# Performance work log

Measured on AMD Instinct MI355X. Metric: run time of the kernel, lower is better.

Reference implementation:

```python
import jax, jax.numpy as jnp
import numpy as np

B, S, F = 4096, 128, 8
H1, H2 = 64, 32


def setup_inputs() -> dict:
    key = jax.random.key(0)
    ks = jax.random.split(key, 12)
    rn = lambda k, shape, scale: jax.random.normal(k, shape, dtype=jnp.float32) * scale
    return {
        "x": rn(ks[0], (B, S, F), 1.0),
        "time": jax.random.uniform(ks[1], (B, 1), dtype=jnp.float32),
        # linear_combine: (S*F + 1) -> S*F
        "W_combine": rn(ks[2], (S * F, S * F + 1), 1.0 / np.sqrt(S * F + 1)),
        "b_combine": jnp.zeros((S * F,), jnp.float32),
        # LSTM layer 1 (bias=False), gate order i,f,g,o like torch
        "W_ih1": rn(ks[3], (4 * H1, F), 1.0 / np.sqrt(H1)),
        "W_hh1": rn(ks[4], (4 * H1, H1), 1.0 / np.sqrt(H1)),
        # LSTM layer 2 (bias=True)
        "W_ih2": rn(ks[5], (4 * H2, H1), 1.0 / np.sqrt(H2)),
        "W_hh2": rn(ks[6], (4 * H2, H2), 1.0 / np.sqrt(H2)),
        "b_ih2": rn(ks[7], (4 * H2,), 0.05),
        "b_hh2": rn(ks[8], (4 * H2,), 0.05),
        # l_linear_supervised: (H2*S) -> 1
        "W_out": rn(ks[9], (1, H2 * S), 1.0 / np.sqrt(H2 * S)),
        "b_out": jnp.zeros((1,), jnp.float32),
    }


def _lstm(x, W_ih, W_hh, b):
    """batch_first LSTM, zero initial state. x: [B,S,D] -> hidden seq [B,S,H]."""
    Bq = x.shape[0]
    H = W_hh.shape[1]
    # precompute input contribution for all timesteps: [B,S,4H]
    xg = jnp.einsum('bsd,gd->bsg', x, W_ih) + b

    def step(carry, xg_t):
        h, c = carry
        g = xg_t + h @ W_hh.T
        i, f, gg, o = jnp.split(g, 4, axis=-1)  # torch gate order i,f,g,o
        c = jax.nn.sigmoid(f) * c + jax.nn.sigmoid(i) * jnp.tanh(gg)
        h = jax.nn.sigmoid(o) * jnp.tanh(c)
        return (h, c), h

    h0 = jnp.zeros((Bq, H), x.dtype)
    (_, _), hs = jax.lax.scan(step, (h0, h0), jnp.swapaxes(xg, 0, 1))
    return jnp.swapaxes(hs, 0, 1)


def reference(x, time, W_combine, b_combine, W_ih1, W_hh1, W_ih2, W_hh2,
              b_ih2, b_hh2, W_out, b_out):
    Bq = x.shape[0]
    # future_time_as_input == 1 branch: flatten, append time, linear + relu
    xf = jnp.concatenate([x.reshape(Bq, -1), time.reshape(Bq, -1)], axis=1)
    xf = jax.nn.relu(xf @ W_combine.T + b_combine)
    x1 = xf.reshape(Bq, S, F)
    h1 = _lstm(x1, W_ih1, W_hh1, jnp.zeros((4 * H1,), x.dtype))  # [B,S,64]
    h2 = _lstm(h1, W_ih2, W_hh2, b_ih2 + b_hh2)                   # [B,S,32]
    return h2.reshape(Bq, -1) @ W_out.T + b_out                   # [B,1]
```

## Files before the change

### kernel.cpp

```cpp
#include <hip/hip_runtime.h>
#include <math.h>


typedef _Float16 f16x8 __attribute__((ext_vector_type(8)));
typedef float f32x4 __attribute__((ext_vector_type(4)));

union H8 { uint4 q; _Float16 h[8]; f16x8 v; };

#define MF(A, B, C) __builtin_amdgcn_mfma_f32_16x16x32_f16(A, B, C, 0, 0, 0)
#define LOG2E 1.44269504f

__device__ __forceinline__ float sigm_pre(float y) {
  return __builtin_amdgcn_rcpf(1.f + __builtin_amdgcn_exp2f(-y));
}
__device__ __forceinline__ float tanh_pre(float y) {
  return 1.f - 2.f * __builtin_amdgcn_rcpf(1.f + __builtin_amdgcn_exp2f(y + y));
}
__device__ __forceinline__ float tanh_raw(float c) {
  return 1.f - 2.f * __builtin_amdgcn_rcpf(1.f + __builtin_amdgcn_exp2f(c * 2.88539008f));
}
__device__ __forceinline__ unsigned pkrtz(float a, float b) {
  return __builtin_bit_cast(unsigned, __builtin_amdgcn_cvt_pkrtz(a, b));
}

#define CROW 72

__global__ __launch_bounds__(256, 2) void combine_mfma(
    const float* __restrict__ x, const float* __restrict__ tme,
    const float* __restrict__ Wc, const float* __restrict__ bc,
    unsigned* __restrict__ x1u)
{
  __shared__ __align__(16) _Float16 sA[128][CROW];
  __shared__ __align__(16) _Float16 sB[64][CROW];
  __shared__ float sT[128];
  __shared__ float sWl[64];
  __shared__ float sBc[64];
  _Float16 (*Cst)[CROW] = sA;

  const int tid = threadIdx.x;
  const int lane = tid & 63;
  const int w = tid >> 6;
  const int r = lane & 15, grp = lane >> 4;
  const int M0 = blockIdx.y * 128, N0 = blockIdx.x * 64;

  if (tid < 128) sT[tid] = tme[M0 + tid];
  else if (tid < 192) sWl[tid - 128] = Wc[(size_t)(N0 + tid - 128) * 1025 + 1024];
  else sBc[tid - 192] = bc[N0 + tid - 192];

  f32x4 acc[2][4];
#pragma unroll
  for (int i = 0; i < 2; ++i)
#pragma unroll
    for (int j = 0; j < 4; ++j) acc[i][j] = f32x4{0.f, 0.f, 0.f, 0.f};

  for (int kt = 0; kt < 1024; kt += 64) {
#pragma unroll
    for (int i = 0; i < 8; ++i) {
      int idx = tid + i * 256;
      int row = idx >> 4, kq = idx & 15;
      float4 v = *(const float4*)&x[(size_t)(M0 + row) * 1024 + kt + kq * 4];
      *(uint2*)&sA[row][kq * 4] = uint2{pkrtz(v.x, v.y), pkrtz(v.z, v.w)};
    }
#pragma unroll
    for (int i = 0; i < 4; ++i) {
      int idx = tid + i * 256;
      int row = idx >> 4, kq = idx & 15;
      float4 v = *(const float4*)&Wc[(size_t)(N0 + row) * 1025 + kt + kq * 4];
      *(uint2*)&sB[row][kq * 4] = uint2{pkrtz(v.x, v.y), pkrtz(v.z, v.w)};
    }
    __syncthreads();

    H8 af[2][2], bf[4][2];
#pragma unroll
    for (int i = 0; i < 2; ++i)
#pragma unroll
      for (int c = 0; c < 2; ++c)
        af[i][c].q = *(const uint4*)&sA[w * 32 + i * 16 + r][c * 32 + grp * 8];
#pragma unroll
    for (int j = 0; j < 4; ++j)
#pragma unroll
      for (int c = 0; c < 2; ++c)
        bf[j][c].q = *(const uint4*)&sB[j * 16 + r][c * 32 + grp * 8];
#pragma unroll
    for (int i = 0; i < 2; ++i)
#pragma unroll
      for (int j = 0; j < 4; ++j) {
        acc[i][j] = MF(af[i][0].v, bf[j][0].v, acc[i][j]);
        acc[i][j] = MF(af[i][1].v, bf[j][1].v, acc[i][j]);
      }
    __syncthreads();
  }

#pragma unroll
  for (int i = 0; i < 2; ++i) {
#pragma unroll
    for (int j = 0; j < 4; ++j) {
      int n = j * 16 + r;
      float wl = sWl[n], bv = sBc[n];
#pragma unroll
      for (int q = 0; q < 4; ++q) {
        int mm = w * 32 + i * 16 + 4 * grp + q;
        float v = acc[i][j][q] + sT[mm] * wl + bv;
        Cst[mm][n] = (_Float16)fmaxf(v, 0.f);
      }
    }
  }
  __syncthreads();
#pragma unroll
  for (int i = 0; i < 4; ++i) {
    int idx = tid + i * 256;
    int row = idx >> 3, c8 = idx & 7;
    uint4 v = *(const uint4*)&Cst[row][c8 * 8];
    *(uint4*)&x1u[(size_t)(M0 + row) * 512 + (N0 >> 1) + c8 * 4] = v;
  }
}

#define ROW1 72
#define ROW2 40

__global__ __launch_bounds__(512, 2) void lstm_fused_mfma(
    const unsigned* __restrict__ x1u,
    const float* __restrict__ Wih1, const float* __restrict__ Whh1,
    const float* __restrict__ Wih2, const float* __restrict__ Whh2,
    const float* __restrict__ bih2, const float* __restrict__ bhh2,
    const float* __restrict__ Wout, const float* __restrict__ bout,
    float* __restrict__ out)
{
  __shared__ __align__(16) unsigned sxw[128 * 16 * 4];
  __shared__ float sWoT[32 * 132];
  __shared__ __align__(16) unsigned short sh1[2][16][ROW1];
  __shared__ __align__(16) unsigned short sh2[2][16][ROW2];
  __shared__ float sOut[8][16];

  const int tid = threadIdx.x;
  const int lane = tid & 63;
  const int w = tid >> 6;
  const int vw = w >> 1;
  const int wsub = w & 1;
  const int col = lane & 15;
  const int grp = lane >> 4;
  const int b0 = blockIdx.x * 16;

  const int m1 = col >> 2, g1 = col & 3;
  f16x8 A1h[2][2];
  f16x8 A1x[2];
#pragma unroll
  for (int jj = 0; jj < 2; ++jj) {
    const int wr = g1 * 64 + vw * 16 + 4 * m1 + (2 * wsub + jj);
#pragma unroll
    for (int c = 0; c < 2; ++c) {
      H8 f;
#pragma unroll
      for (int q = 0; q < 8; ++q)
        f.h[q] = (_Float16)(Whh1[wr * 64 + c * 32 + grp * 8 + q] * LOG2E);
      A1h[jj][c] = f.v;
    }
    H8 fx;
#pragma unroll
    for (int q = 0; q < 8; ++q)
      fx.h[q] = (grp == 0) ? (_Float16)(Wih1[wr * 8 + q] * LOG2E) : (_Float16)0.f;
    A1x[jj] = fx.v;
  }
  f16x8 A2[3];
  const int u = 2 * vw + wsub;
  {
    const int wr = g1 * 32 + 4 * u + m1;
#pragma unroll
    for (int c = 0; c < 3; ++c) {
      H8 f;
#pragma unroll
      for (int q = 0; q < 8; ++q) {
        float wv = (c < 2) ? Wih2[wr * 64 + c * 32 + grp * 8 + q]
                           : Whh2[wr * 32 + grp * 8 + q];
        f.h[q] = (_Float16)(wv * LOG2E);
      }
      A2[c] = f.v;
    }
  }
  const int h2o = 4 * u + grp;
  f32x4 b2q;
#pragma unroll
  for (int r = 0; r < 4; ++r)
    b2q[r] = (bih2[r * 32 + h2o] + bhh2[r * 32 + h2o]) * LOG2E;
  const f32x4 zq = {0.f, 0.f, 0.f, 0.f};

  for (int idx = tid; idx < 4096; idx += 512) {
    int t = idx >> 5, h = idx & 31;
    sWoT[h * 132 + t] = Wout[idx];
  }
  {
    unsigned short* z = &sh1[0][0][0];
    for (int i2 = tid; i2 < 2 * 16 * ROW1; i2 += 512) z[i2] = 0;
    unsigned short* z2 = &sh2[0][0][0];
    for (int i2 = tid; i2 < 2 * 16 * ROW2; i2 += 512) z2[i2] = 0;
  }
  for (int idx = tid; idx < 16 * 512; idx += 512) {
    int bb = idx >> 9, rem = idx & 511;
    int t = rem >> 2, pr = rem & 3;
    sxw[t * 64 + bb * 4 + pr] = x1u[(size_t)(b0 + bb) * 512 + rem];
  }
  __syncthreads();

  float c1a = 0.f, c1b = 0.f, c2 = 0.f, accO = 0.f;

#define PHASE(T, CUR, DO_L1, DO_L2)                                            \
  {                                                                            \
    H8 s0, s1, s2;                                                             \
    s0.q = *(const uint4*)&sh1[CUR][col][grp * 8];                             \
    s1.q = *(const uint4*)&sh1[CUR][col][32 + grp * 8];                        \
    s2.q = *(const uint4*)&sh2[CUR][col][grp * 8];                             \
    if (DO_L2) {                                                               \
      const float won = sWoT[h2o * 132 + (T) - 1];                             \
      f32x4 a = MF(A2[2], s2.v, b2q);                                          \
      a = MF(A2[0], s0.v, a);                                                  \
      a = MF(A2[1], s1.v, a);                                                  \
      float ig = sigm_pre(a[0]), fg = sigm_pre(a[1]);                          \
      float tg = tanh_pre(a[2]), og = sigm_pre(a[3]);                          \
      float cc = fg * c2 + ig * tg;                                            \
      c2 = cc;                                                                 \
      float hn = og * tanh_raw(cc);                                            \
      accO = fmaf(hn, won, accO);                                              \
      *(_Float16*)&sh2[(CUR) ^ 1][col][h2o] = (_Float16)hn;                    \
    }                                                                          \
    if (DO_L1) {                                                               \
      H8 sx;                                                                   \
      sx.q = *(const uint4*)&sxw[(T) * 64 + col * 4];                          \
      f32x4 a0 = MF(A1x[0], sx.v, zq);                                         \
      f32x4 a1 = MF(A1x[1], sx.v, zq);                                         \
      a0 = MF(A1h[0][0], s0.v, a0);                                            \
      a1 = MF(A1h[1][0], s0.v, a1);                                            \
      a0 = MF(A1h[0][1], s1.v, a0);                                            \
      a1 = MF(A1h[1][1], s1.v, a1);                                            \
      float ig0 = sigm_pre(a0[0]), fg0 = sigm_pre(a0[1]);                      \
      float tg0 = tanh_pre(a0[2]), og0 = sigm_pre(a0[3]);                      \
      float cc0 = fg0 * c1a + ig0 * tg0;                                       \
      c1a = cc0;                                                               \
      float h0 = og0 * tanh_raw(cc0);                                          \
      float ig1 = sigm_pre(a1[0]), fg1 = sigm_pre(a1[1]);                      \
      float tg1 = tanh_pre(a1[2]), og1 = sigm_pre(a1[3]);                      \
      float cc1 = fg1 * c1b + ig1 * tg1;                                       \
      c1b = cc1;                                                               \
      float h1v = og1 * tanh_raw(cc1);                                         \
      *(unsigned*)&sh1[(CUR) ^ 1][col][vw * 16 + 4 * grp + 2 * wsub] =         \
          pkrtz(h0, h1v);                                                      \
    }                                                                          \
    __syncthreads();                                                           \
  }

  PHASE(0, 0, true, false);
  PHASE(1, 1, true, true);
  for (int tt = 1; tt < 64; ++tt) {
    const int t0 = 2 * tt;
    PHASE(t0, 0, true, true);
    PHASE(t0 + 1, 1, true, true);
  }
  PHASE(128, 0, false, true);
#undef PHASE

  accO += __shfl_xor(accO, 16);
  accO += __shfl_xor(accO, 32);
  if (grp == 0) sOut[u][col] = accO;
  __syncthreads();
  if (tid < 16) {
    float s = bout[0];
#pragma unroll
    for (int q = 0; q < 8; ++q) s += sOut[q][tid];
    out[b0 + tid] = s;
  }
}

extern "C" void kernel_launch(void* const* d_in, const int* in_sizes, int n_in,
                              void* d_out, int out_size, void* d_ws, size_t ws_size,
                              hipStream_t stream) {
  const float* x    = (const float*)d_in[0];
  const float* tme  = (const float*)d_in[1];
  const float* Wc   = (const float*)d_in[2];
  const float* bc   = (const float*)d_in[3];
  const float* Wih1 = (const float*)d_in[4];
  const float* Whh1 = (const float*)d_in[5];
  const float* Wih2 = (const float*)d_in[6];
  const float* Whh2 = (const float*)d_in[7];
  const float* bih2 = (const float*)d_in[8];
  const float* bhh2 = (const float*)d_in[9];
  const float* Wout = (const float*)d_in[10];
  const float* bout = (const float*)d_in[11];
  float* outp = (float*)d_out;
  unsigned* x1u = (unsigned*)d_ws;

  dim3 gA(16, 32);
  combine_mfma<<<gA, 256, 0, stream>>>(x, tme, Wc, bc, x1u);
  lstm_fused_mfma<<<256, 512, 0, stream>>>(x1u, Wih1, Whh1, Wih2, Whh2,
                                           bih2, bhh2, Wout, bout, outp);
}
```

Baseline: 105.7 us.

## Pre-convert x to fp16, double-buffer combine GEMM, fold tanh doubling into weights

```diff
diff --git a/kernel.cpp b/kernel.cpp
--- a/kernel.cpp
+++ b/kernel.cpp
@@ -13,8 +13,8 @@
 __device__ __forceinline__ float sigm_pre(float y) {
   return __builtin_amdgcn_rcpf(1.f + __builtin_amdgcn_exp2f(-y));
 }
-__device__ __forceinline__ float tanh_pre(float y) {
-  return 1.f - 2.f * __builtin_amdgcn_rcpf(1.f + __builtin_amdgcn_exp2f(y + y));
+__device__ __forceinline__ float tanh_pre2(float y2) {
+  return 1.f - 2.f * __builtin_amdgcn_rcpf(1.f + __builtin_amdgcn_exp2f(y2));
 }
 __device__ __forceinline__ float tanh_raw(float c) {
   return 1.f - 2.f * __builtin_amdgcn_rcpf(1.f + __builtin_amdgcn_exp2f(c * 2.88539008f));
@@ -23,19 +23,29 @@
   return __builtin_bit_cast(unsigned, __builtin_amdgcn_cvt_pkrtz(a, b));
 }
 
+__global__ __launch_bounds__(256) void cvt_x(
+    const float* __restrict__ x, unsigned* __restrict__ x16)
+{
+  const int idx = blockIdx.x * 256 + threadIdx.x;
+  const float4* src = (const float4*)x;
+  float4 a = src[2 * idx], b = src[2 * idx + 1];
+  uint4 o = {pkrtz(a.x, a.y), pkrtz(a.z, a.w), pkrtz(b.x, b.y), pkrtz(b.z, b.w)};
+  ((uint4*)x16)[idx] = o;
+}
+
 #define CROW 72
 
 __global__ __launch_bounds__(256, 2) void combine_mfma(
-    const float* __restrict__ x, const float* __restrict__ tme,
+    const _Float16* __restrict__ xh, const float* __restrict__ tme,
     const float* __restrict__ Wc, const float* __restrict__ bc,
     unsigned* __restrict__ x1u)
 {
-  __shared__ __align__(16) _Float16 sA[128][CROW];
-  __shared__ __align__(16) _Float16 sB[64][CROW];
+  __shared__ __align__(16) _Float16 sA[2][128][CROW];
+  __shared__ __align__(16) _Float16 sB[2][64][CROW];
   __shared__ float sT[128];
   __shared__ float sWl[64];
   __shared__ float sBc[64];
-  _Float16 (*Cst)[CROW] = sA;
+  _Float16 (*Cst)[CROW] = sA[0];
 
   const int tid = threadIdx.x;
   const int lane = tid & 63;
@@ -47,40 +57,50 @@
   else if (tid < 192) sWl[tid - 128] = Wc[(size_t)(N0 + tid - 128) * 1025 + 1024];
   else sBc[tid - 192] = bc[N0 + tid - 192];
 
+#define STAGE_A(KT, BUF)                                                       \
+  _Pragma("unroll") for (int i = 0; i < 4; ++i) {                              \
+    int idx = tid + i * 256;                                                   \
+    int row = idx >> 3, kq = idx & 7;                                          \
+    uint4 v = *(const uint4*)&xh[(size_t)(M0 + row) * 1024 + (KT) + kq * 8];   \
+    *(uint4*)&sA[BUF][row][kq * 8] = v;                                        \
+  }
+#define STAGE_B(KT, BUF)                                                       \
+  _Pragma("unroll") for (int i = 0; i < 4; ++i) {                              \
+    int idx = tid + i * 256;                                                   \
+    int row = idx >> 4, kq = idx & 15;                                         \
+    float4 v = *(const float4*)&Wc[(size_t)(N0 + row) * 1025 + (KT) + kq * 4]; \
+    *(uint2*)&sB[BUF][row][kq * 4] = uint2{pkrtz(v.x, v.y), pkrtz(v.z, v.w)};  \
+  }
+
   f32x4 acc[2][4];
 #pragma unroll
   for (int i = 0; i < 2; ++i)
 #pragma unroll
     for (int j = 0; j < 4; ++j) acc[i][j] = f32x4{0.f, 0.f, 0.f, 0.f};
 
+  STAGE_A(0, 0);
+  STAGE_B(0, 0);
+  __syncthreads();
+
+  int cur = 0;
   for (int kt = 0; kt < 1024; kt += 64) {
-#pragma unroll
-    for (int i = 0; i < 8; ++i) {
-      int idx = tid + i * 256;
-      int row = idx >> 4, kq = idx & 15;
-      float4 v = *(const float4*)&x[(size_t)(M0 + row) * 1024 + kt + kq * 4];
-      *(uint2*)&sA[row][kq * 4] = uint2{pkrtz(v.x, v.y), pkrtz(v.z, v.w)};
+    H8 af[2][2], bf[4][2];
+#pragma unroll
+    for (int i = 0; i < 2; ++i)
+#pragma unroll
+      for (int c = 0; c < 2; ++c)
+        af[i][c].q = *(const uint4*)&sA[cur][w * 32 + i * 16 + r][c * 32 + grp * 8];
+#pragma unroll
+    for (int j = 0; j < 4; ++j)
+#pragma unroll
+      for (int c = 0; c < 2; ++c)
+        bf[j][c].q = *(const uint4*)&sB[cur][j * 16 + r][c * 32 + grp * 8];
+
+    if (kt < 960) {
+      STAGE_A(kt + 64, cur ^ 1);
+      STAGE_B(kt + 64, cur ^ 1);
     }
-#pragma unroll
-    for (int i = 0; i < 4; ++i) {
-      int idx = tid + i * 256;
-      int row = idx >> 4, kq = idx & 15;
-      float4 v = *(const float4*)&Wc[(size_t)(N0 + row) * 1025 + kt + kq * 4];
-      *(uint2*)&sB[row][kq * 4] = uint2{pkrtz(v.x, v.y), pkrtz(v.z, v.w)};
-    }
-    __syncthreads();
-
-    H8 af[2][2], bf[4][2];
-#pragma unroll
-    for (int i = 0; i < 2; ++i)
-#pragma unroll
-      for (int c = 0; c < 2; ++c)
-        af[i][c].q = *(const uint4*)&sA[w * 32 + i * 16 + r][c * 32 + grp * 8];
-#pragma unroll
-    for (int j = 0; j < 4; ++j)
-#pragma unroll
-      for (int c = 0; c < 2; ++c)
-        bf[j][c].q = *(const uint4*)&sB[j * 16 + r][c * 32 + grp * 8];
+
 #pragma unroll
     for (int i = 0; i < 2; ++i)
 #pragma unroll
@@ -89,7 +109,10 @@
         acc[i][j] = MF(af[i][1].v, bf[j][1].v, acc[i][j]);
       }
     __syncthreads();
-  }
+    cur ^= 1;
+  }
+#undef STAGE_A
+#undef STAGE_B
 
 #pragma unroll
   for (int i = 0; i < 2; ++i) {
@@ -142,6 +165,7 @@
   const int b0 = blockIdx.x * 16;
 
   const int m1 = col >> 2, g1 = col & 3;
+  const float gsc = (g1 == 2) ? 2.f * LOG2E : LOG2E;
   f16x8 A1h[2][2];
   f16x8 A1x[2];
 #pragma unroll
@@ -152,13 +176,13 @@
       H8 f;
 #pragma unroll
       for (int q = 0; q < 8; ++q)
-        f.h[q] = (_Float16)(Whh1[wr * 64 + c * 32 + grp * 8 + q] * LOG2E);
+        f.h[q] = (_Float16)(Whh1[wr * 64 + c * 32 + grp * 8 + q] * gsc);
       A1h[jj][c] = f.v;
     }
     H8 fx;
 #pragma unroll
     for (int q = 0; q < 8; ++q)
-      fx.h[q] = (grp == 0) ? (_Float16)(Wih1[wr * 8 + q] * LOG2E) : (_Float16)0.f;
+      fx.h[q] = (grp == 0) ? (_Float16)(Wih1[wr * 8 + q] * gsc) : (_Float16)0.f;
     A1x[jj] = fx.v;
   }
   f16x8 A2[3];
@@ -172,7 +196,7 @@
       for (int q = 0; q < 8; ++q) {
         float wv = (c < 2) ? Wih2[wr * 64 + c * 32 + grp * 8 + q]
                            : Whh2[wr * 32 + grp * 8 + q];
-        f.h[q] = (_Float16)(wv * LOG2E);
+        f.h[q] = (_Float16)(wv * gsc);
       }
       A2[c] = f.v;
     }
@@ -180,8 +204,10 @@
   const int h2o = 4 * u + grp;
   f32x4 b2q;
 #pragma unroll
-  for (int r = 0; r < 4; ++r)
-    b2q[r] = (bih2[r * 32 + h2o] + bhh2[r * 32 + h2o]) * LOG2E;
+  for (int r = 0; r < 4; ++r) {
+    const float rs = (r == 2) ? 2.f * LOG2E : LOG2E;
+    b2q[r] = (bih2[r * 32 + h2o] + bhh2[r * 32 + h2o]) * rs;
+  }
   const f32x4 zq = {0.f, 0.f, 0.f, 0.f};
 
   for (int idx = tid; idx < 4096; idx += 512) {
@@ -215,7 +241,7 @@
       a = MF(A2[0], s0.v, a);                                                  \
       a = MF(A2[1], s1.v, a);                                                  \
       float ig = sigm_pre(a[0]), fg = sigm_pre(a[1]);                          \
-      float tg = tanh_pre(a[2]), og = sigm_pre(a[3]);                          \
+      float tg = tanh_pre2(a[2]), og = sigm_pre(a[3]);                         \
       float cc = fg * c2 + ig * tg;                                            \
       c2 = cc;                                                                 \
       float hn = og * tanh_raw(cc);                                            \
@@ -232,12 +258,12 @@
       a0 = MF(A1h[0][1], s1.v, a0);                                            \
       a1 = MF(A1h[1][1], s1.v, a1);                                            \
       float ig0 = sigm_pre(a0[0]), fg0 = sigm_pre(a0[1]);                      \
-      float tg0 = tanh_pre(a0[2]), og0 = sigm_pre(a0[3]);                      \
+      float tg0 = tanh_pre2(a0[2]), og0 = sigm_pre(a0[3]);                     \
       float cc0 = fg0 * c1a + ig0 * tg0;                                       \
       c1a = cc0;                                                               \
       float h0 = og0 * tanh_raw(cc0);                                          \
       float ig1 = sigm_pre(a1[0]), fg1 = sigm_pre(a1[1]);                      \
-      float tg1 = tanh_pre(a1[2]), og1 = sigm_pre(a1[3]);                      \
+      float tg1 = tanh_pre2(a1[2]), og1 = sigm_pre(a1[3]);                     \
       float cc1 = fg1 * c1b + ig1 * tg1;                                       \
       c1b = cc1;                                                               \
       float h1v = og1 * tanh_raw(cc1);                                         \
@@ -286,9 +312,11 @@
   const float* bout = (const float*)d_in[11];
   float* outp = (float*)d_out;
   unsigned* x1u = (unsigned*)d_ws;
-
+  unsigned* x16 = x1u + (size_t)4096 * 512;
+
+  cvt_x<<<2048, 256, 0, stream>>>(x, x16);
   dim3 gA(16, 32);
-  combine_mfma<<<gA, 256, 0, stream>>>(x, tme, Wc, bc, x1u);
+  combine_mfma<<<gA, 256, 0, stream>>>((const _Float16*)x16, tme, Wc, bc, x1u);
   lstm_fused_mfma<<<256, 512, 0, stream>>>(x1u, Wih1, Whh1, Wih2, Whh2,
                                            bih2, bhh2, Wout, bout, outp);
 }
```

New measurement: 106.0 us. No clear change (+0.3%).
